# Kernel optimization log

Measured on AMD Instinct MI355X. Metric: run time of the kernel, lower is better.

The kernel has to match this reference:

```python
import jax, jax.numpy as jnp
import numpy as np

B, L, K, M, N, P, D = 8, 512, 512, 64, 64, 64, 64  # M == D required for residual add


def _layernorm(x, gamma, beta, eps=1e-3):  # keras LayerNormalization default eps
    mu = jnp.mean(x, axis=-1, keepdims=True)
    var = jnp.var(x, axis=-1, keepdims=True)
    return (x - mu) * jax.lax.rsqrt(var + eps) * gamma + beta


def setup_inputs() -> dict:
    key = jax.random.key(0)
    ks = jax.random.split(key, 5)
    return {
        "q": jax.random.normal(ks[0], (B, L, D), dtype=jnp.float32),
        "k": jax.random.normal(ks[1], (B, K, D), dtype=jnp.float32),
        "vq": jax.random.normal(ks[2], (B, L, M, N), dtype=jnp.float32),
        "vk": jax.random.normal(ks[3], (B, K, P, N), dtype=jnp.float32),
        "vexp": jax.random.normal(ks[4], (B, K, P), dtype=jnp.float32),
        "scale": jnp.ones((), dtype=jnp.float32),      # keras Attention use_scale param (init 1)
        "ln_gamma": jnp.ones((D,), dtype=jnp.float32),  # LayerNormalization gamma
        "ln_beta": jnp.zeros((D,), dtype=jnp.float32),  # LayerNormalization beta
    }


def reference(q, k, vq, vk, vexp, scale, ln_gamma, ln_beta):
    # scores: keras Attention with use_scale -> scale * q @ k^T  (B, L, K)
    scores = scale * jnp.einsum('bld,bkd->blk', q, k)
    # no mask in this call path; plain softmax over keys
    weights = jax.nn.softmax(scores, axis=-1)

    # Original value path (materializes 5D 'blkmp'):
    #   s1 = einsum('blmn,bkpn->blkmp', vq, vk)
    #   v  = einsum('blkmp,bkp->blkm', s1, vexp)
    #   out = einsum('blk,blkm->blm', weights, v)
    # Mathematically identical reassociation that never builds the 5D tensor:
    vkc = jnp.einsum('bkpn,bkp->bkn', vk, vexp)       # contract P first
    tmp = jnp.einsum('blk,bkn->bln', weights, vkc)    # softmax-weighted combine over K
    attn_out = jnp.einsum('blmn,bln->blm', vq, tmp)   # contract N -> (B, L, M)

    # BaseAttentionCell / CrossAttention: residual add + LayerNorm
    return _layernorm(q + attn_out, ln_gamma, ln_beta)
```

## Files before the change

kernel.cpp:

```cpp
#include <hip/hip_runtime.h>


__global__ __launch_bounds__(256) void vkc_kernel(const float* __restrict__ vk,
                                                  const float* __restrict__ vexp,
                                                  float* __restrict__ vkc) {
    const int wave = (blockIdx.x << 2) + (threadIdx.x >> 6);
    const int lane = threadIdx.x & 63;

    const float ve_reg = vexp[wave * 64 + lane];
    const int n0 = (lane & 15) << 2;
    const float* base = vk + (long)wave * 4096;

    float ax = 0.f, ay = 0.f, az = 0.f, aw = 0.f;
    #pragma unroll
    for (int it = 0; it < 16; ++it) {
        const int p = (lane >> 4) + (it << 2);
        const float4 v4 = *(const float4*)(base + p * 64 + n0);
        const float w = __shfl(ve_reg, p, 64);
        ax += v4.x * w; ay += v4.y * w; az += v4.z * w; aw += v4.w * w;
    }
    ax += __shfl_down(ax, 32, 64); ax += __shfl_down(ax, 16, 64);
    ay += __shfl_down(ay, 32, 64); ay += __shfl_down(ay, 16, 64);
    az += __shfl_down(az, 32, 64); az += __shfl_down(az, 16, 64);
    aw += __shfl_down(aw, 32, 64); aw += __shfl_down(aw, 16, 64);

    if ((lane & 48) == 0) {
        float4 r; r.x = ax; r.y = ay; r.z = az; r.w = aw;
        *(float4*)(vkc + wave * 64 + n0) = r;
    }
}

__global__ __launch_bounds__(512) void attn_kernel(const float* __restrict__ q,
                                                   const float* __restrict__ k,
                                                   const float* __restrict__ vq,
                                                   const float* __restrict__ vkc,
                                                   const float* __restrict__ scale_p,
                                                   const float* __restrict__ gamma,
                                                   const float* __restrict__ beta,
                                                   float* __restrict__ out) {
    __shared__ float q_s[8 * 64];
    __shared__ float sc[8][512];
    __shared__ float tp[8][8][64];
    __shared__ float tmp_s[8 * 64];
    __shared__ float attn_s[8][64];

    const int t = threadIdx.x;
    const int wv = t >> 6;
    const int lane = t & 63;
    const int batch = blockIdx.x >> 6;
    const int l0 = (blockIdx.x & 63) << 3;

    const float scale = scale_p[0];

    q_s[t] = q[(batch * 512 + l0) * 64 + t];
    __syncthreads();

    {
        const float4* krow = (const float4*)(k + (batch * 512 + t) * 64);
        const float4* q4 = (const float4*)q_s;
        float acc[8] = {0.f, 0.f, 0.f, 0.f, 0.f, 0.f, 0.f, 0.f};
        #pragma unroll
        for (int dc = 0; dc < 16; ++dc) {
            const float4 kv = krow[dc];
            #pragma unroll
            for (int l = 0; l < 8; ++l) {
                const float4 p = q4[l * 16 + dc];
                acc[l] += p.x * kv.x + p.y * kv.y + p.z * kv.z + p.w * kv.w;
            }
        }
        #pragma unroll
        for (int l = 0; l < 8; ++l) sc[l][t] = scale * acc[l];
    }
    __syncthreads();

    {
        float v[8]; float mx = -1e30f;
        #pragma unroll
        for (int j = 0; j < 8; ++j) { v[j] = sc[wv][lane + 64 * j]; mx = fmaxf(mx, v[j]); }
        #pragma unroll
        for (int off = 32; off; off >>= 1) mx = fmaxf(mx, __shfl_xor(mx, off, 64));
        float s = 0.f;
        #pragma unroll
        for (int j = 0; j < 8; ++j) { v[j] = __expf(v[j] - mx); s += v[j]; }
        #pragma unroll
        for (int off = 32; off; off >>= 1) s += __shfl_xor(s, off, 64);
        const float inv = 1.0f / s;
        #pragma unroll
        for (int j = 0; j < 8; ++j) sc[wv][lane + 64 * j] = v[j] * inv;
    }
    __syncthreads();

    {
        const float* vkcb = vkc + batch * 512 * 64;
        const int ksub = lane >> 4;
        const int n0 = (lane & 15) << 2;
        const int kbeg = wv << 6;
        float4 a[8];
        #pragma unroll
        for (int l = 0; l < 8; ++l) { a[l].x = 0.f; a[l].y = 0.f; a[l].z = 0.f; a[l].w = 0.f; }
        #pragma unroll
        for (int i = 0; i < 16; ++i) {
            const int kk = kbeg + (i << 2) + ksub;
            const float4 v4 = *(const float4*)(vkcb + kk * 64 + n0);
            #pragma unroll
            for (int l = 0; l < 8; ++l) {
                const float w = sc[l][kk];
                a[l].x += w * v4.x; a[l].y += w * v4.y;
                a[l].z += w * v4.z; a[l].w += w * v4.w;
            }
        }
        #pragma unroll
        for (int l = 0; l < 8; ++l) {
            a[l].x += __shfl_down(a[l].x, 32, 64); a[l].x += __shfl_down(a[l].x, 16, 64);
            a[l].y += __shfl_down(a[l].y, 32, 64); a[l].y += __shfl_down(a[l].y, 16, 64);
            a[l].z += __shfl_down(a[l].z, 32, 64); a[l].z += __shfl_down(a[l].z, 16, 64);
            a[l].w += __shfl_down(a[l].w, 32, 64); a[l].w += __shfl_down(a[l].w, 16, 64);
        }
        if (lane < 16) {
            #pragma unroll
            for (int l = 0; l < 8; ++l)
                *(float4*)&tp[wv][l][lane << 2] = a[l];
        }
    }
    __syncthreads();
    {
        float s = tp[0][wv][lane];
        #pragma unroll
        for (int w = 1; w < 8; ++w) s += tp[w][wv][lane];
        tmp_s[t] = s;
    }
    __syncthreads();

    {
        const float* vql = vq + (long)(batch * 512 + l0 + wv) * 4096;
        const int n0 = (lane & 15) << 2;
        const float4 t4 = *(const float4*)&tmp_s[wv * 64 + n0];
        #pragma unroll
        for (int it = 0; it < 16; ++it) {
            const float4 v4 = *(const float4*)(vql + it * 256 + lane * 4);
            float part = v4.x * t4.x + v4.y * t4.y + v4.z * t4.z + v4.w * t4.w;
            part += __shfl_down(part, 8, 16);
            part += __shfl_down(part, 4, 16);
            part += __shfl_down(part, 2, 16);
            part += __shfl_down(part, 1, 16);
            if ((lane & 15) == 0) attn_s[wv][it * 4 + (lane >> 4)] = part;
        }
    }

    {
        const float x = q_s[wv * 64 + lane] + attn_s[wv][lane];
        float s1 = x, s2 = x * x;
        #pragma unroll
        for (int off = 32; off; off >>= 1) {
            s1 += __shfl_xor(s1, off, 64);
            s2 += __shfl_xor(s2, off, 64);
        }
        const float mean = s1 * (1.0f / 64.0f);
        const float var = s2 * (1.0f / 64.0f) - mean * mean;
        const float r = rsqrtf(var + 1e-3f);
        out[(batch * 512 + l0 + wv) * 64 + lane] =
            (x - mean) * r * gamma[lane] + beta[lane];
    }
}

extern "C" void kernel_launch(void* const* d_in, const int* in_sizes, int n_in,
                              void* d_out, int out_size, void* d_ws, size_t ws_size,
                              hipStream_t stream) {
    const float* q     = (const float*)d_in[0];
    const float* k     = (const float*)d_in[1];
    const float* vq    = (const float*)d_in[2];
    const float* vk    = (const float*)d_in[3];
    const float* vexp  = (const float*)d_in[4];
    const float* scale = (const float*)d_in[5];
    const float* gamma = (const float*)d_in[6];
    const float* beta  = (const float*)d_in[7];
    float* out = (float*)d_out;
    float* vkc = (float*)d_ws;

    vkc_kernel<<<1024, 256, 0, stream>>>(vk, vexp, vkc);
    attn_kernel<<<512, 512, 0, stream>>>(q, k, vq, vkc, scale, gamma, beta, out);
}
```

Before: 186.1 us.

## Split attention kernel so vq streaming runs in a separate high-occupancy kernel

```diff
diff --git a/kernel.cpp b/kernel.cpp
--- a/kernel.cpp
+++ b/kernel.cpp
@@ -30,19 +30,14 @@
     }
 }
 
-__global__ __launch_bounds__(512) void attn_kernel(const float* __restrict__ q,
-                                                   const float* __restrict__ k,
-                                                   const float* __restrict__ vq,
-                                                   const float* __restrict__ vkc,
-                                                   const float* __restrict__ scale_p,
-                                                   const float* __restrict__ gamma,
-                                                   const float* __restrict__ beta,
-                                                   float* __restrict__ out) {
+__global__ __launch_bounds__(512) void score_tmp_kernel(const float* __restrict__ q,
+                                                        const float* __restrict__ k,
+                                                        const float* __restrict__ vkc,
+                                                        const float* __restrict__ scale_p,
+                                                        float* __restrict__ tmp_g) {
     __shared__ float q_s[8 * 64];
     __shared__ float sc[8][512];
     __shared__ float tp[8][8][64];
-    __shared__ float tmp_s[8 * 64];
-    __shared__ float attn_s[8][64];
 
     const int t = threadIdx.x;
     const int wv = t >> 6;
@@ -127,40 +122,54 @@
         float s = tp[0][wv][lane];
         #pragma unroll
         for (int w = 1; w < 8; ++w) s += tp[w][wv][lane];
-        tmp_s[t] = s;
+        tmp_g[(batch * 512 + l0) * 64 + t] = s;
     }
-    __syncthreads();
+}
 
-    {
-        const float* vql = vq + (long)(batch * 512 + l0 + wv) * 4096;
-        const int n0 = (lane & 15) << 2;
-        const float4 t4 = *(const float4*)&tmp_s[wv * 64 + n0];
-        #pragma unroll
-        for (int it = 0; it < 16; ++it) {
-            const float4 v4 = *(const float4*)(vql + it * 256 + lane * 4);
-            float part = v4.x * t4.x + v4.y * t4.y + v4.z * t4.z + v4.w * t4.w;
-            part += __shfl_down(part, 8, 16);
-            part += __shfl_down(part, 4, 16);
-            part += __shfl_down(part, 2, 16);
-            part += __shfl_down(part, 1, 16);
-            if ((lane & 15) == 0) attn_s[wv][it * 4 + (lane >> 4)] = part;
-        }
+__global__ __launch_bounds__(256) void out_kernel(const float* __restrict__ q,
+                                                  const float* __restrict__ vq,
+                                                  const float* __restrict__ tmp_g,
+                                                  const float* __restrict__ gamma,
+                                                  const float* __restrict__ beta,
+                                                  float* __restrict__ out) {
+    __shared__ float attn_s[4][64];
+
+    const int wv = threadIdx.x >> 6;
+    const int lane = threadIdx.x & 63;
+    const int row = (blockIdx.x << 2) + wv;
+
+    const float* vql = vq + (long)row * 4096;
+
+    float4 v[16];
+    #pragma unroll
+    for (int it = 0; it < 16; ++it)
+        v[it] = *(const float4*)(vql + it * 256 + lane * 4);
+
+    const float qv = q[row * 64 + lane];
+    const int n0 = (lane & 15) << 2;
+    const float4 t4 = *(const float4*)(tmp_g + row * 64 + n0);
+
+    #pragma unroll
+    for (int it = 0; it < 16; ++it) {
+        float part = v[it].x * t4.x + v[it].y * t4.y + v[it].z * t4.z + v[it].w * t4.w;
+        part += __shfl_down(part, 8, 16);
+        part += __shfl_down(part, 4, 16);
+        part += __shfl_down(part, 2, 16);
+        part += __shfl_down(part, 1, 16);
+        if ((lane & 15) == 0) attn_s[wv][it * 4 + (lane >> 4)] = part;
     }
 
-    {
-        const float x = q_s[wv * 64 + lane] + attn_s[wv][lane];
-        float s1 = x, s2 = x * x;
-        #pragma unroll
-        for (int off = 32; off; off >>= 1) {
-            s1 += __shfl_xor(s1, off, 64);
-            s2 += __shfl_xor(s2, off, 64);
-        }
-        const float mean = s1 * (1.0f / 64.0f);
-        const float var = s2 * (1.0f / 64.0f) - mean * mean;
-        const float r = rsqrtf(var + 1e-3f);
-        out[(batch * 512 + l0 + wv) * 64 + lane] =
-            (x - mean) * r * gamma[lane] + beta[lane];
+    const float x = qv + attn_s[wv][lane];
+    float s1 = x, s2 = x * x;
+    #pragma unroll
+    for (int off = 32; off; off >>= 1) {
+        s1 += __shfl_xor(s1, off, 64);
+        s2 += __shfl_xor(s2, off, 64);
     }
+    const float mean = s1 * (1.0f / 64.0f);
+    const float var = s2 * (1.0f / 64.0f) - mean * mean;
+    const float r = rsqrtf(var + 1e-3f);
+    out[row * 64 + lane] = (x - mean) * r * gamma[lane] + beta[lane];
 }
 
 extern "C" void kernel_launch(void* const* d_in, const int* in_sizes, int n_in,
@@ -175,8 +184,11 @@
     const float* gamma = (const float*)d_in[6];
     const float* beta  = (const float*)d_in[7];
     float* out = (float*)d_out;
+
     float* vkc = (float*)d_ws;
+    float* tmp = vkc + 8 * 512 * 64;
 
     vkc_kernel<<<1024, 256, 0, stream>>>(vk, vexp, vkc);
-    attn_kernel<<<512, 512, 0, stream>>>(q, k, vq, vkc, scale, gamma, beta, out);
+    score_tmp_kernel<<<512, 512, 0, stream>>>(q, k, vkc, scale, tmp);
+    out_kernel<<<1024, 256, 0, stream>>>(q, vq, tmp, gamma, beta, out);
 }
```

Result: no change. 186.5 us (+0.2%).

## Move scores and softmax into the vkc pre-pass and shrink attention blocks

Applied to the files above, without the earlier changes.

```diff
diff --git a/kernel.cpp b/kernel.cpp
--- a/kernel.cpp
+++ b/kernel.cpp
@@ -1,92 +1,119 @@
 #include <hip/hip_runtime.h>
 
 
-__global__ __launch_bounds__(256) void vkc_kernel(const float* __restrict__ vk,
+__global__ __launch_bounds__(256) void pre_kernel(const float* __restrict__ q,
+                                                  const float* __restrict__ k,
+                                                  const float* __restrict__ vk,
                                                   const float* __restrict__ vexp,
-                                                  float* __restrict__ vkc) {
-    const int wave = (blockIdx.x << 2) + (threadIdx.x >> 6);
-    const int lane = threadIdx.x & 63;
-
-    const float ve_reg = vexp[wave * 64 + lane];
-    const int n0 = (lane & 15) << 2;
-    const float* base = vk + (long)wave * 4096;
-
-    float ax = 0.f, ay = 0.f, az = 0.f, aw = 0.f;
-    #pragma unroll
-    for (int it = 0; it < 16; ++it) {
-        const int p = (lane >> 4) + (it << 2);
-        const float4 v4 = *(const float4*)(base + p * 64 + n0);
-        const float w = __shfl(ve_reg, p, 64);
-        ax += v4.x * w; ay += v4.y * w; az += v4.z * w; aw += v4.w * w;
-    }
-    ax += __shfl_down(ax, 32, 64); ax += __shfl_down(ax, 16, 64);
-    ay += __shfl_down(ay, 32, 64); ay += __shfl_down(ay, 16, 64);
-    az += __shfl_down(az, 32, 64); az += __shfl_down(az, 16, 64);
-    aw += __shfl_down(aw, 32, 64); aw += __shfl_down(aw, 16, 64);
-
-    if ((lane & 48) == 0) {
-        float4 r; r.x = ax; r.y = ay; r.z = az; r.w = aw;
-        *(float4*)(vkc + wave * 64 + n0) = r;
+                                                  const float* __restrict__ scale_p,
+                                                  float* __restrict__ vkc,
+                                                  float* __restrict__ wts) {
+    __shared__ float q_s[4 * 64];
+    __shared__ float sc[4][512];
+
+    const int t = threadIdx.x;
+    const int wv = t >> 6;
+    const int lane = t & 63;
+    const int batch = blockIdx.x >> 7;
+    const int l0 = (blockIdx.x & 127) << 2;
+
+    const float scale = scale_p[0];
+
+    q_s[t] = q[(batch * 512 + l0) * 64 + t];
+
+    {
+        const int row = (blockIdx.x << 2) + wv;
+        const float ve = vexp[row * 64 + lane];
+        const int n0 = (lane & 15) << 2;
+        const float* base = vk + (long)row * 4096;
+        float ax = 0.f, ay = 0.f, az = 0.f, aw = 0.f;
+        #pragma unroll
+        for (int it = 0; it < 16; ++it) {
+            const int p = (lane >> 4) + (it << 2);
+            const float4 v4 = *(const float4*)(base + p * 64 + n0);
+            const float w = __shfl(ve, p, 64);
+            ax += v4.x * w; ay += v4.y * w; az += v4.z * w; aw += v4.w * w;
+        }
+        ax += __shfl_down(ax, 32, 64); ax += __shfl_down(ax, 16, 64);
+        ay += __shfl_down(ay, 32, 64); ay += __shfl_down(ay, 16, 64);
+        az += __shfl_down(az, 32, 64); az += __shfl_down(az, 16, 64);
+        aw += __shfl_down(aw, 32, 64); aw += __shfl_down(aw, 16, 64);
+        if ((lane & 48) == 0) {
+            float4 r; r.x = ax; r.y = ay; r.z = az; r.w = aw;
+            *(float4*)(vkc + row * 64 + n0) = r;
+        }
+    }
+    __syncthreads();
+
+    {
+        const float* kb = k + batch * 512 * 64;
+        const float4* q4 = (const float4*)q_s;
+        #pragma unroll
+        for (int rep = 0; rep < 2; ++rep) {
+            const int kk = t + (rep << 8);
+            const float4* krow = (const float4*)(kb + kk * 64);
+            float a0 = 0.f, a1 = 0.f, a2 = 0.f, a3 = 0.f;
+            #pragma unroll
+            for (int dc = 0; dc < 16; ++dc) {
+                const float4 kv = krow[dc];
+                const float4 p0 = q4[dc];
+                const float4 p1 = q4[16 + dc];
+                const float4 p2 = q4[32 + dc];
+                const float4 p3 = q4[48 + dc];
+                a0 += p0.x * kv.x + p0.y * kv.y + p0.z * kv.z + p0.w * kv.w;
+                a1 += p1.x * kv.x + p1.y * kv.y + p1.z * kv.z + p1.w * kv.w;
+                a2 += p2.x * kv.x + p2.y * kv.y + p2.z * kv.z + p2.w * kv.w;
+                a3 += p3.x * kv.x + p3.y * kv.y + p3.z * kv.z + p3.w * kv.w;
+            }
+            sc[0][kk] = scale * a0;
+            sc[1][kk] = scale * a1;
+            sc[2][kk] = scale * a2;
+            sc[3][kk] = scale * a3;
+        }
+    }
+    __syncthreads();
+
+    {
+        float v[8]; float mx = -1e30f;
+        #pragma unroll
+        for (int j = 0; j < 8; ++j) { v[j] = sc[wv][lane + 64 * j]; mx = fmaxf(mx, v[j]); }
+        #pragma unroll
+        for (int off = 32; off; off >>= 1) mx = fmaxf(mx, __shfl_xor(mx, off, 64));
+        float s = 0.f;
+        #pragma unroll
+        for (int j = 0; j < 8; ++j) { v[j] = __expf(v[j] - mx); s += v[j]; }
+        #pragma unroll
+        for (int off = 32; off; off >>= 1) s += __shfl_xor(s, off, 64);
+        const float inv = 1.0f / s;
+        float* wrow = wts + (long)(batch * 512 + l0 + wv) * 512;
+        #pragma unroll
+        for (int j = 0; j < 8; ++j) wrow[lane + 64 * j] = v[j] * inv;
     }
 }
 
-__global__ __launch_bounds__(512) void attn_kernel(const float* __restrict__ q,
-                                                   const float* __restrict__ k,
+__global__ __launch_bounds__(256) void post_kernel(const float* __restrict__ q,
                                                    const float* __restrict__ vq,
                                                    const float* __restrict__ vkc,
-                                                   const float* __restrict__ scale_p,
+                                                   const float* __restrict__ wts,
                                                    const float* __restrict__ gamma,
                                                    const float* __restrict__ beta,
                                                    float* __restrict__ out) {
-    __shared__ float q_s[8 * 64];
-    __shared__ float sc[8][512];
-    __shared__ float tp[8][8][64];
-    __shared__ float tmp_s[8 * 64];
-    __shared__ float attn_s[8][64];
+    __shared__ float w_s[4 * 512];
+    __shared__ float tp[4][4][64];
+    __shared__ float tmp_s[4 * 64];
+    __shared__ float attn_s[4][64];
 
     const int t = threadIdx.x;
     const int wv = t >> 6;
     const int lane = t & 63;
-    const int batch = blockIdx.x >> 6;
-    const int l0 = (blockIdx.x & 63) << 3;
-
-    const float scale = scale_p[0];
-
-    q_s[t] = q[(batch * 512 + l0) * 64 + t];
-    __syncthreads();
-
-    {
-        const float4* krow = (const float4*)(k + (batch * 512 + t) * 64);
-        const float4* q4 = (const float4*)q_s;
-        float acc[8] = {0.f, 0.f, 0.f, 0.f, 0.f, 0.f, 0.f, 0.f};
-        #pragma unroll
-        for (int dc = 0; dc < 16; ++dc) {
-            const float4 kv = krow[dc];
-            #pragma unroll
-            for (int l = 0; l < 8; ++l) {
-                const float4 p = q4[l * 16 + dc];
-                acc[l] += p.x * kv.x + p.y * kv.y + p.z * kv.z + p.w * kv.w;
-            }
-        }
-        #pragma unroll
-        for (int l = 0; l < 8; ++l) sc[l][t] = scale * acc[l];
-    }
-    __syncthreads();
-
-    {
-        float v[8]; float mx = -1e30f;
-        #pragma unroll
-        for (int j = 0; j < 8; ++j) { v[j] = sc[wv][lane + 64 * j]; mx = fmaxf(mx, v[j]); }
-        #pragma unroll
-        for (int off = 32; off; off >>= 1) mx = fmaxf(mx, __shfl_xor(mx, off, 64));
-        float s = 0.f;
-        #pragma unroll
-        for (int j = 0; j < 8; ++j) { v[j] = __expf(v[j] - mx); s += v[j]; }
-        #pragma unroll
-        for (int off = 32; off; off >>= 1) s += __shfl_xor(s, off, 64);
-        const float inv = 1.0f / s;
-        #pragma unroll
-        for (int j = 0; j < 8; ++j) sc[wv][lane + 64 * j] = v[j] * inv;
+    const int batch = blockIdx.x >> 7;
+    const int l0 = (blockIdx.x & 127) << 2;
+
+    {
+        const float* wg = wts + (long)(batch * 512 + l0) * 512;
+        #pragma unroll
+        for (int i = 0; i < 2; ++i)
+            *(float4*)(w_s + t * 4 + i * 1024) = *(const float4*)(wg + t * 4 + i * 1024);
     }
     __syncthreads();
 
@@ -94,23 +121,23 @@
         const float* vkcb = vkc + batch * 512 * 64;
         const int ksub = lane >> 4;
         const int n0 = (lane & 15) << 2;
-        const int kbeg = wv << 6;
-        float4 a[8];
-        #pragma unroll
-        for (int l = 0; l < 8; ++l) { a[l].x = 0.f; a[l].y = 0.f; a[l].z = 0.f; a[l].w = 0.f; }
-        #pragma unroll
-        for (int i = 0; i < 16; ++i) {
+        const int kbeg = wv << 7;
+        float4 a[4];
+        #pragma unroll
+        for (int l = 0; l < 4; ++l) { a[l].x = 0.f; a[l].y = 0.f; a[l].z = 0.f; a[l].w = 0.f; }
+        #pragma unroll 8
+        for (int i = 0; i < 32; ++i) {
             const int kk = kbeg + (i << 2) + ksub;
             const float4 v4 = *(const float4*)(vkcb + kk * 64 + n0);
             #pragma unroll
-            for (int l = 0; l < 8; ++l) {
-                const float w = sc[l][kk];
+            for (int l = 0; l < 4; ++l) {
+                const float w = w_s[l * 512 + kk];
                 a[l].x += w * v4.x; a[l].y += w * v4.y;
                 a[l].z += w * v4.z; a[l].w += w * v4.w;
             }
         }
         #pragma unroll
-        for (int l = 0; l < 8; ++l) {
+        for (int l = 0; l < 4; ++l) {
             a[l].x += __shfl_down(a[l].x, 32, 64); a[l].x += __shfl_down(a[l].x, 16, 64);
             a[l].y += __shfl_down(a[l].y, 32, 64); a[l].y += __shfl_down(a[l].y, 16, 64);
             a[l].z += __shfl_down(a[l].z, 32, 64); a[l].z += __shfl_down(a[l].z, 16, 64);
@@ -118,16 +145,14 @@
         }
         if (lane < 16) {
             #pragma unroll
-            for (int l = 0; l < 8; ++l)
+            for (int l = 0; l < 4; ++l)
                 *(float4*)&tp[wv][l][lane << 2] = a[l];
         }
     }
     __syncthreads();
     {
-        float s = tp[0][wv][lane];
-        #pragma unroll
-        for (int w = 1; w < 8; ++w) s += tp[w][wv][lane];
-        tmp_s[t] = s;
+        const int l = t >> 6, n = t & 63;
+        tmp_s[t] = tp[0][l][n] + tp[1][l][n] + tp[2][l][n] + tp[3][l][n];
     }
     __syncthreads();
 
@@ -148,7 +173,8 @@
     }
 
     {
-        const float x = q_s[wv * 64 + lane] + attn_s[wv][lane];
+        const int row = batch * 512 + l0 + wv;
+        const float x = q[row * 64 + lane] + attn_s[wv][lane];
         float s1 = x, s2 = x * x;
         #pragma unroll
         for (int off = 32; off; off >>= 1) {
@@ -158,8 +184,7 @@
         const float mean = s1 * (1.0f / 64.0f);
         const float var = s2 * (1.0f / 64.0f) - mean * mean;
         const float r = rsqrtf(var + 1e-3f);
-        out[(batch * 512 + l0 + wv) * 64 + lane] =
-            (x - mean) * r * gamma[lane] + beta[lane];
+        out[row * 64 + lane] = (x - mean) * r * gamma[lane] + beta[lane];
     }
 }
 
@@ -175,8 +200,10 @@
     const float* gamma = (const float*)d_in[6];
     const float* beta  = (const float*)d_in[7];
     float* out = (float*)d_out;
+
     float* vkc = (float*)d_ws;
-
-    vkc_kernel<<<1024, 256, 0, stream>>>(vk, vexp, vkc);
-    attn_kernel<<<512, 512, 0, stream>>>(q, k, vq, vkc, scale, gamma, beta, out);
+    float* wts = vkc + 8 * 512 * 64;
+
+    pre_kernel<<<1024, 256, 0, stream>>>(q, k, vk, vexp, scale, vkc, wts);
+    post_kernel<<<1024, 256, 0, stream>>>(q, vq, vkc, wts, gamma, beta, out);
 }
```

Measured after the change: 203.0 us. 1.09x slower.
